# Kernel optimization log

Hardware: AMD Instinct MI355X
Metric: run time of the kernel (lower is better)

## Reference

```python
import jax, jax.numpy as jnp
import numpy as np

DIM = 1024
HEADS = 16
HEAD_DIM = DIM // HEADS
B, S = 4, 4096


def setup_inputs() -> dict:
    key = jax.random.key(0)
    ks = jax.random.split(key, 8)
    sc = 1.0 / np.sqrt(DIM)
    return {
        "x": jax.random.normal(ks[0], (B, S, DIM), dtype=jnp.float32),
        "Wq": jax.random.normal(ks[1], (DIM, DIM), dtype=jnp.float32) * sc,
        "Wk": jax.random.normal(ks[2], (DIM, DIM), dtype=jnp.float32) * sc,
        "Wv": jax.random.normal(ks[3], (DIM, DIM), dtype=jnp.float32) * sc,
        "Wp": jax.random.normal(ks[4], (DIM, DIM), dtype=jnp.float32) * sc,
        "bp": jnp.zeros((DIM,), dtype=jnp.float32),
        "conv_w": jax.random.normal(ks[5], (DIM, 3), dtype=jnp.float32) * (1.0 / np.sqrt(3.0)),
        "conv_b": jnp.zeros((DIM,), dtype=jnp.float32),
    }


def reference(x, Wq, Wk, Wv, Wp, bp, conv_w, conv_b):
    b, s, d = x.shape
    # projections -> [b, h, n, hd] (torch Linear: x @ W.T)
    def split_heads(t):
        return t.reshape(b, s, HEADS, HEAD_DIM).transpose(0, 2, 1, 3)
    q = split_heads(x @ Wq.T)
    k = split_heads(x @ Wk.T)
    v = split_heads(x @ Wv.T)
    # ELU(+1) feature map
    q = jax.nn.elu(q) + 1.0
    k = jax.nn.elu(k) + 1.0
    # global kv-state and k-state
    kv_state = jnp.einsum('bhnd,bhne->bhde', k, v)   # [b,h,hd,hd]
    k_state = k.sum(axis=2)                          # [b,h,hd]
    attn_out = jnp.einsum('bhnd,bhde->bhne', q, kv_state)
    denom = jnp.maximum(jnp.einsum('bhnd,bhd->bhn', q, k_state), 1e-6)[..., None]
    attn_out = (attn_out / denom).transpose(0, 2, 1, 3).reshape(b, s, d)
    # depthwise conv1d, kernel=3, padding=1 (per-channel)
    xp = jnp.pad(x, ((0, 0), (1, 1), (0, 0)))        # [b, s+2, d]
    local = (xp[:, :-2, :] * conv_w[:, 0]
             + xp[:, 1:-1, :] * conv_w[:, 1]
             + xp[:, 2:, :] * conv_w[:, 2]) + conv_b
    return (attn_out + local) @ Wp.T + bp
```

## Files before the change

kernel.cpp:

```cpp
#include <hip/hip_runtime.h>
#include <hip/hip_bf16.h>
#include <stdint.h>

#define DIMN 1024
#define HEADS 16
#define HD 64
#define BATCH 4
#define SEQ 4096
#define M_TOT (BATCH*SEQ)

typedef __attribute__((ext_vector_type(8))) __bf16 bf16x8;
typedef __attribute__((ext_vector_type(4))) __bf16 bf16x4;
typedef __attribute__((ext_vector_type(4))) float f32x4;

__device__ __forceinline__ void gload_lds16(const void* g, void* l) {
  __builtin_amdgcn_global_load_lds(
      (const __attribute__((address_space(1))) void*)(uintptr_t)g,
      (__attribute__((address_space(3))) void*)(uint32_t)(uintptr_t)l,
      16, 0, 0);
}

__device__ __forceinline__ uint32_t swz128(uint32_t off) {
  return off ^ (((off >> 7) & 7) << 4);
}

__device__ __forceinline__ void lfence() { asm volatile("" ::: "memory"); }
__device__ __forceinline__ void barx() { lfence(); __builtin_amdgcn_s_barrier(); lfence(); }

__global__ __launch_bounds__(256) void cast_x_kernel(const float* __restrict__ in,
                                                     __bf16* __restrict__ out, int n4) {
  int i = blockIdx.x * 256 + threadIdx.x;
  if (i < n4) {
    f32x4 v = ((const f32x4*)in)[i];
    bf16x4 o;
    o[0] = (__bf16)v[0]; o[1] = (__bf16)v[1]; o[2] = (__bf16)v[2]; o[3] = (__bf16)v[3];
    ((bf16x4*)out)[i] = o;
  }
}

__global__ __launch_bounds__(256) void cast_w4_kernel(const float* __restrict__ a,
                                                      const float* __restrict__ b,
                                                      const float* __restrict__ c,
                                                      const float* __restrict__ d,
                                                      __bf16* __restrict__ oa,
                                                      __bf16* __restrict__ ob,
                                                      __bf16* __restrict__ oc,
                                                      __bf16* __restrict__ od) {
  const float* srcs[4] = {a, b, c, d};
  __bf16* dsts[4] = {oa, ob, oc, od};
  const float* src = srcs[blockIdx.y];
  __bf16* dst = dsts[blockIdx.y];
  int i = blockIdx.x * 256 + threadIdx.x;
  f32x4 v = ((const f32x4*)src)[i];
  bf16x4 o;
  o[0] = (__bf16)v[0]; o[1] = (__bf16)v[1]; o[2] = (__bf16)v[2]; o[3] = (__bf16)v[3];
  ((bf16x4*)dst)[i] = o;
}

template <int MODE, int NT>
__global__ __launch_bounds__(512, 2) void gemm256(const __bf16* __restrict__ A,
                                                  const __bf16* __restrict__ Bw,
                                                  void* __restrict__ Cout,
                                                  const float* __restrict__ bias) {
  __shared__ char lds[131072];
  const int KB = DIMN * 2;
  const int NKT = DIMN / 64;
  const int bid = blockIdx.x;
  const int x = bid & 7, jj = bid >> 3;
  const int n_t = jj % NT, m_t = (jj / NT) * 8 + x;
  const int m0 = m_t * 256, n0 = n_t * 256;
  const int tid = threadIdx.x;
  const int lane = tid & 63;
  const int wave = tid >> 6;
  const int wm = wave >> 2;
  const int wn = wave & 3;
  const int r16 = lane & 15, r4 = lane >> 4;

  const uint32_t s_off0 = tid * 16;
  const uint32_t s_off1 = 8192 + tid * 16;
  const uint32_t s_row0 = s_off0 >> 7, s_row1 = s_off1 >> 7;
  const uint32_t s_col0 = (s_off0 ^ ((s_row0 & 7) << 4)) & 127;
  const uint32_t s_col1 = (s_off1 ^ ((s_row1 & 7) << 4)) & 127;

  const char* Ab = (const char*)A + (size_t)m0 * KB;
  const char* Bb = (const char*)Bw + (size_t)n0 * KB;

  auto STAGE = [&](int op, int h, int kt, int b) {
    const char* gb = (op ? Bb : Ab) + (size_t)(h * 128) * KB + kt * 128;
    char* lb = lds + op * 65536 + b * 32768 + h * 16384;
    gload_lds16(gb + s_row0 * KB + s_col0, lb + s_off0);
    gload_lds16(gb + s_row1 * KB + s_col1, lb + s_off1);
  };

  uint32_t axk[2];
#pragma unroll
  for (int k = 0; k < 2; ++k) axk[k] = (uint32_t)(k * 64 + r4 * 16) ^ ((r16 & 7) << 4);

  f32x4 acc[8][4] = {};
  bf16x8 bc[4][2];

  STAGE(1, 0, 0, 0); STAGE(1, 1, 0, 0); STAGE(0, 0, 0, 0); STAGE(0, 1, 0, 0);
  STAGE(1, 0, 1, 1); STAGE(1, 1, 1, 1); STAGE(0, 0, 1, 1);
  asm volatile("s_waitcnt vmcnt(6)" ::: "memory");
  barx();

  for (int kt = 0; kt < NKT; ++kt) {
    const int p = kt & 1;
    const char* abuf = lds + p * 32768;
    const char* bbuf = lds + 65536 + p * 32768;

    {
      bf16x8 af[2][2];
#pragma unroll
      for (int nf = 0; nf < 4; ++nf)
#pragma unroll
        for (int k = 0; k < 2; ++k)
          bc[nf][k] = *(const bf16x8*)(bbuf + (nf >> 1) * 16384 +
                        (((nf & 1) * 64 + wn * 16 + r16) << 7) + axk[k]);
#pragma unroll
      for (int i = 0; i < 2; ++i)
#pragma unroll
        for (int k = 0; k < 2; ++k)
          af[i][k] = *(const bf16x8*)(abuf + ((i * 32 + wm * 16 + r16) << 7) + axk[k]);
      if (kt + 1 < NKT) STAGE(0, 1, kt + 1, (kt + 1) & 1);
      barx();
      __builtin_amdgcn_s_setprio(1);
#pragma unroll
      for (int i = 0; i < 2; ++i)
#pragma unroll
        for (int nf = 0; nf < 4; ++nf)
#pragma unroll
          for (int k = 0; k < 2; ++k)
            acc[i][nf] = __builtin_amdgcn_mfma_f32_16x16x32_bf16(af[i][k], bc[nf][k], acc[i][nf], 0, 0, 0);
      __builtin_amdgcn_s_setprio(0);
      barx();
    }
    {
      bf16x8 af[2][2];
#pragma unroll
      for (int i = 0; i < 2; ++i)
#pragma unroll
        for (int k = 0; k < 2; ++k)
          af[i][k] = *(const bf16x8*)(abuf + (((2 + i) * 32 + wm * 16 + r16) << 7) + axk[k]);
      if (kt + 2 < NKT) STAGE(1, 0, kt + 2, p);
      barx();
      __builtin_amdgcn_s_setprio(1);
#pragma unroll
      for (int i = 0; i < 2; ++i)
#pragma unroll
        for (int nf = 0; nf < 4; ++nf)
#pragma unroll
          for (int k = 0; k < 2; ++k)
            acc[2 + i][nf] = __builtin_amdgcn_mfma_f32_16x16x32_bf16(af[i][k], bc[nf][k], acc[2 + i][nf], 0, 0, 0);
      __builtin_amdgcn_s_setprio(0);
      barx();
    }
    {
      bf16x8 af[2][2];
#pragma unroll
      for (int i = 0; i < 2; ++i)
#pragma unroll
        for (int k = 0; k < 2; ++k)
          af[i][k] = *(const bf16x8*)(abuf + 16384 + ((i * 32 + wm * 16 + r16) << 7) + axk[k]);
      if (kt + 2 < NKT) STAGE(1, 1, kt + 2, p);
      barx();
      __builtin_amdgcn_s_setprio(1);
#pragma unroll
      for (int i = 0; i < 2; ++i)
#pragma unroll
        for (int nf = 0; nf < 4; ++nf)
#pragma unroll
          for (int k = 0; k < 2; ++k)
            acc[4 + i][nf] = __builtin_amdgcn_mfma_f32_16x16x32_bf16(af[i][k], bc[nf][k], acc[4 + i][nf], 0, 0, 0);
      __builtin_amdgcn_s_setprio(0);
      barx();
    }
    {
      bf16x8 af[2][2];
#pragma unroll
      for (int i = 0; i < 2; ++i)
#pragma unroll
        for (int k = 0; k < 2; ++k)
          af[i][k] = *(const bf16x8*)(abuf + 16384 + (((2 + i) * 32 + wm * 16 + r16) << 7) + axk[k]);
      if (kt + 2 < NKT) STAGE(0, 0, kt + 2, p);
      if (kt == NKT - 2) { asm volatile("s_waitcnt vmcnt(0)" ::: "memory"); }
      else if (kt < NKT - 2) { asm volatile("s_waitcnt vmcnt(6)" ::: "memory"); }
      barx();
      __builtin_amdgcn_s_setprio(1);
#pragma unroll
      for (int i = 0; i < 2; ++i)
#pragma unroll
        for (int nf = 0; nf < 4; ++nf)
#pragma unroll
          for (int k = 0; k < 2; ++k)
            acc[6 + i][nf] = __builtin_amdgcn_mfma_f32_16x16x32_bf16(af[i][k], bc[nf][k], acc[6 + i][nf], 0, 0, 0);
      __builtin_amdgcn_s_setprio(0);
      barx();
    }
  }

#pragma unroll
  for (int mf = 0; mf < 8; ++mf) {
#pragma unroll
    for (int nf = 0; nf < 4; ++nf) {
#pragma unroll
      for (int r = 0; r < 4; ++r) {
        int row = m0 + mf * 32 + wm * 16 + r4 * 4 + r;
        int col = n0 + nf * 64 + wn * 16 + r16;
        float v = acc[mf][nf][r];
        if (MODE == 2) {
          ((float*)Cout)[(size_t)row * DIMN + col] = v + bias[col];
        } else {
          int wsel = col >> 10, c = col & 1023;
          if (wsel < 2) v = (v > 0.f) ? (v + 1.f) : __expf(v);
          int b = row >> 12, s = row & 4095;
          int h = c >> 6, e2 = c & 63;
          ((__bf16*)Cout)[(size_t)wsel * 16777216 +
                          ((size_t)((b * HEADS + h) * SEQ + s)) * HD + e2] = (__bf16)v;
        }
      }
    }
  }
}

__global__ __launch_bounds__(256) void kv_state_mfma(const __bf16* __restrict__ kp,
                                                     const __bf16* __restrict__ vb,
                                                     float* __restrict__ kv,
                                                     float* __restrict__ ks) {
  __shared__ __bf16 kt[64][136];
  __shared__ __bf16 vt[80][136];
  const int bid = blockIdx.x;
  const int bh = bid >> 2, nc = bid & 3;
  const int tid = threadIdx.x;
  const int lane = tid & 63;
  const int wave = tid >> 6;
  const int r16 = lane & 15, r4 = lane >> 4;

  for (int i = tid; i < 16 * 136; i += 256) {
    int rr = i / 136;
    vt[64 + rr][i - rr * 136] = (rr == 0) ? (__bf16)1.0f : (__bf16)0.0f;
  }

  const int trow = tid >> 1;
  const int tcol = (tid & 1) * 32;

  f32x4 acc[5] = {};
  bf16x8 kr[4], vr[4];

  size_t gb = ((size_t)bh * SEQ + nc * 1024 + trow) * HD + tcol;
#pragma unroll
  for (int q = 0; q < 4; ++q) {
    kr[q] = *(const bf16x8*)(kp + gb + q * 8);
    vr[q] = *(const bf16x8*)(vb + gb + q * 8);
  }

  for (int t = 0; t < 8; ++t) {
    __syncthreads();
#pragma unroll
    for (int q = 0; q < 4; ++q)
#pragma unroll
      for (int j = 0; j < 8; ++j) {
        kt[tcol + q * 8 + j][trow] = kr[q][j];
        vt[tcol + q * 8 + j][trow] = vr[q][j];
      }
    __syncthreads();
    if (t < 7) {
      size_t gb2 = ((size_t)bh * SEQ + nc * 1024 + (t + 1) * 128 + trow) * HD + tcol;
#pragma unroll
      for (int q = 0; q < 4; ++q) {
        kr[q] = *(const bf16x8*)(kp + gb2 + q * 8);
        vr[q] = *(const bf16x8*)(vb + gb2 + q * 8);
      }
    }
#pragma unroll
    for (int ksl = 0; ksl < 4; ++ksl) {
      bf16x8 af = *(const bf16x8*)&kt[wave * 16 + r16][ksl * 32 + r4 * 8];
#pragma unroll
      for (int eb = 0; eb < 5; ++eb) {
        bf16x8 bf_ = *(const bf16x8*)&vt[eb * 16 + r16][ksl * 32 + r4 * 8];
        acc[eb] = __builtin_amdgcn_mfma_f32_16x16x32_bf16(af, bf_, acc[eb], 0, 0, 0);
      }
    }
  }

#pragma unroll
  for (int eb = 0; eb < 4; ++eb)
#pragma unroll
    for (int r = 0; r < 4; ++r) {
      int d = wave * 16 + r4 * 4 + r;
      atomicAdd(&kv[(size_t)bh * 4096 + d * 64 + eb * 16 + r16], acc[eb][r]);
    }
  if (r16 == 0) {
#pragma unroll
    for (int r = 0; r < 4; ++r)
      atomicAdd(&ks[bh * 64 + wave * 16 + r4 * 4 + r], acc[4][r]);
  }
}

__global__ __launch_bounds__(256) void prep_kv_kernel(const float* __restrict__ kv,
                                                      const float* __restrict__ ks,
                                                      __bf16* __restrict__ kvb) {
  const int bh = blockIdx.x;
  const int tid = threadIdx.x;
  for (int idx = tid; idx < 80 * 64; idx += 256) {
    int e = idx >> 6, d = idx & 63;
    float v;
    if (e < 64)       v = kv[(size_t)bh * 4096 + d * 64 + e];
    else if (e == 64) v = ks[bh * 64 + d];
    else              v = 0.f;
    kvb[(size_t)bh * 5120 + idx] = (__bf16)v;
  }
}

__global__ __launch_bounds__(256) void attn_local_mfma(const __bf16* __restrict__ qp,
                                                       const __bf16* __restrict__ kvb,
                                                       const float* __restrict__ x,
                                                       const float* __restrict__ conv_w,
                                                       const float* __restrict__ conv_b,
                                                       __bf16* __restrict__ y) {
  __shared__ __bf16 qs[128 * 64];
  __shared__ __bf16 bs[80 * 64];
  const int bid = blockIdx.x;
  const int bh = bid >> 5;
  const int chunk = bid & 31;
  const int tid = threadIdx.x;
  const int lane = tid & 63;
  const int wave = tid >> 6;
  const int r16 = lane & 15, r4 = lane >> 4;

  const char* qbase  = (const char*)(qp + ((size_t)bh * SEQ + chunk * 128) * HD);
  const char* kvbase = (const char*)(kvb + (size_t)bh * 5120);
#pragma unroll
  for (int t = 0; t < 4; ++t) {
    int c = t * 4 + wave;
    uint32_t off = c * 1024 + lane * 16;
    gload_lds16(qbase + swz128(off), ((char*)qs) + off);
  }
#pragma unroll
  for (int t = 0; t < 3; ++t) {
    int c = t * 4 + wave;
    if (c < 10) {
      uint32_t off = c * 1024 + lane * 16;
      gload_lds16(kvbase + swz128(off), ((char*)bs) + off);
    }
  }
  __syncthreads();

  f32x4 acc[2][5] = {};
#pragma unroll
  for (int kstep = 0; kstep < 2; ++kstep) {
    bf16x8 af[2], bfr[5];
#pragma unroll
    for (int i = 0; i < 2; ++i) {
      uint32_t off = (wave * 32 + i * 16 + r16) * 128 + kstep * 64 + r4 * 16;
      af[i] = *(const bf16x8*)(((char*)qs) + swz128(off));
    }
#pragma unroll
    for (int j = 0; j < 5; ++j) {
      uint32_t off = (j * 16 + r16) * 128 + kstep * 64 + r4 * 16;
      bfr[j] = *(const bf16x8*)(((char*)bs) + swz128(off));
    }
#pragma unroll
    for (int i = 0; i < 2; ++i)
#pragma unroll
      for (int j = 0; j < 5; ++j)
        acc[i][j] = __builtin_amdgcn_mfma_f32_16x16x32_bf16(af[i], bfr[j], acc[i][j], 0, 0, 0);
  }

  const int b = bh >> 4, h = bh & 15;
  float w0[4], w1[4], w2[4], bb[4];
#pragma unroll
  for (int j = 0; j < 4; ++j) {
    int c = h * HD + j * 16 + r16;
    w0[j] = conv_w[c * 3 + 0]; w1[j] = conv_w[c * 3 + 1]; w2[j] = conv_w[c * 3 + 2];
    bb[j] = conv_b[c];
  }
#pragma unroll
  for (int i = 0; i < 2; ++i) {
#pragma unroll
    for (int r = 0; r < 4; ++r) {
      int s = chunk * 128 + wave * 32 + i * 16 + r4 * 4 + r;
      size_t m = (size_t)b * SEQ + s;
      float den = fmaxf(__shfl(acc[i][4][r], lane & 48), 1e-6f);
      float inv = 1.0f / den;
#pragma unroll
      for (int j = 0; j < 4; ++j) {
        int c = h * HD + j * 16 + r16;
        float xm = x[m * DIMN + c];
        float xl = (s > 0)       ? x[(m - 1) * DIMN + c] : 0.f;
        float xr = (s < SEQ - 1) ? x[(m + 1) * DIMN + c] : 0.f;
        float val = acc[i][j][r] * inv
                  + xl * w0[j] + xm * w1[j] + xr * w2[j] + bb[j];
        y[m * DIMN + c] = (__bf16)val;
      }
    }
  }
}

extern "C" void kernel_launch(void* const* d_in, const int* in_sizes, int n_in,
                              void* d_out, int out_size, void* d_ws, size_t ws_size,
                              hipStream_t stream) {
  const float* x  = (const float*)d_in[0];
  const float* Wq = (const float*)d_in[1];
  const float* Wk = (const float*)d_in[2];
  const float* Wv = (const float*)d_in[3];
  const float* Wp = (const float*)d_in[4];
  const float* bp = (const float*)d_in[5];
  const float* cw = (const float*)d_in[6];
  const float* cb = (const float*)d_in[7];
  float* out = (float*)d_out;

  char* ws = (char*)d_ws;
  const size_t MB = 1024 * 1024;
  __bf16* xb  = (__bf16*)(ws);
  __bf16* y   = xb;
  __bf16* qp  = (__bf16*)(ws + 32 * MB);
  __bf16* kp  = (__bf16*)(ws + 64 * MB);
  __bf16* vb  = (__bf16*)(ws + 96 * MB);
  __bf16* wqb = (__bf16*)(ws + 128 * MB);
  __bf16* wkb = (__bf16*)(ws + 130 * MB);
  __bf16* wvb = (__bf16*)(ws + 132 * MB);
  __bf16* wpb = (__bf16*)(ws + 134 * MB);
  float*  kv  = (float*)(ws + 136 * MB);
  float*  ks  = (float*)(ws + 137 * MB);
  __bf16* kvb = wqb;

  cast_x_kernel<<<M_TOT * DIMN / 4 / 256, 256, 0, stream>>>(x, xb, M_TOT * DIMN / 4);
  cast_w4_kernel<<<dim3(1024, 4), 256, 0, stream>>>(Wq, Wk, Wv, Wp, wqb, wkb, wvb, wpb);

  gemm256<3, 12><<<768, 512, 0, stream>>>(xb, wqb, qp, nullptr);

  hipMemsetAsync(kv, 0, 64 * 4096 * 4 + 64 * 64 * 4, stream);
  kv_state_mfma<<<256, 256, 0, stream>>>(kp, vb, kv, ks);
  prep_kv_kernel<<<64, 256, 0, stream>>>(kv, ks, kvb);

  attn_local_mfma<<<2048, 256, 0, stream>>>(qp, kvb, x, cw, cb, y);

  gemm256<2, 4><<<256, 512, 0, stream>>>(y, wpb, out, bp);
}
```

Baseline: 234.4 us.

## Swap MFMA operands for vectorized row-major epilogue stores and merge cast kernels

The GEMM MFMA operands are swapped so each lane's four accumulator values lie along consecutive output columns rather than rows. The epilogue can then write them as one 16-byte float4 store (with a vector bias load) or an 8-byte bf16x4 store, instead of four scalar stores. The ELU selection is hoisted to a per-tile check. Separately, the x and four weight cast kernels are merged into one launch to cut a kernel launch. Correctness depends on the transposed accumulator layout matching the new index math.

Result: slower. 241.5 us (+3.0%).

```diff
diff --git a/kernel.cpp b/kernel.cpp
--- a/kernel.cpp
+++ b/kernel.cpp
@@ -27,34 +27,31 @@
 __device__ __forceinline__ void lfence() { asm volatile("" ::: "memory"); }
 __device__ __forceinline__ void barx() { lfence(); __builtin_amdgcn_s_barrier(); lfence(); }
 
-__global__ __launch_bounds__(256) void cast_x_kernel(const float* __restrict__ in,
-                                                     __bf16* __restrict__ out, int n4) {
+__global__ __launch_bounds__(256) void cast_all_kernel(const float* __restrict__ x,
+                                                       const float* __restrict__ wq,
+                                                       const float* __restrict__ wk,
+                                                       const float* __restrict__ wv,
+                                                       const float* __restrict__ wp,
+                                                       __bf16* __restrict__ xb,
+                                                       __bf16* __restrict__ wqb,
+                                                       __bf16* __restrict__ wkb,
+                                                       __bf16* __restrict__ wvb,
+                                                       __bf16* __restrict__ wpb) {
   int i = blockIdx.x * 256 + threadIdx.x;
-  if (i < n4) {
-    f32x4 v = ((const f32x4*)in)[i];
-    bf16x4 o;
-    o[0] = (__bf16)v[0]; o[1] = (__bf16)v[1]; o[2] = (__bf16)v[2]; o[3] = (__bf16)v[3];
-    ((bf16x4*)out)[i] = o;
-  }
-}
-
-__global__ __launch_bounds__(256) void cast_w4_kernel(const float* __restrict__ a,
-                                                      const float* __restrict__ b,
-                                                      const float* __restrict__ c,
-                                                      const float* __restrict__ d,
-                                                      __bf16* __restrict__ oa,
-                                                      __bf16* __restrict__ ob,
-                                                      __bf16* __restrict__ oc,
-                                                      __bf16* __restrict__ od) {
-  const float* srcs[4] = {a, b, c, d};
-  __bf16* dsts[4] = {oa, ob, oc, od};
-  const float* src = srcs[blockIdx.y];
-  __bf16* dst = dsts[blockIdx.y];
-  int i = blockIdx.x * 256 + threadIdx.x;
-  f32x4 v = ((const f32x4*)src)[i];
+  const float* src; __bf16* dst; int j;
+  if (i < 4194304)      { src = x;  dst = xb;  j = i; }
+  else {
+    int t = i - 4194304;
+    int w = t >> 18; j = t & 262143;
+    if      (w == 0) { src = wq; dst = wqb; }
+    else if (w == 1) { src = wk; dst = wkb; }
+    else if (w == 2) { src = wv; dst = wvb; }
+    else             { src = wp; dst = wpb; }
+  }
+  f32x4 v = ((const f32x4*)src)[j];
   bf16x4 o;
   o[0] = (__bf16)v[0]; o[1] = (__bf16)v[1]; o[2] = (__bf16)v[2]; o[3] = (__bf16)v[3];
-  ((bf16x4*)dst)[i] = o;
+  ((bf16x4*)dst)[j] = o;
 }
 
 template <int MODE, int NT>
@@ -131,7 +128,7 @@
         for (int nf = 0; nf < 4; ++nf)
 #pragma unroll
           for (int k = 0; k < 2; ++k)
-            acc[i][nf] = __builtin_amdgcn_mfma_f32_16x16x32_bf16(af[i][k], bc[nf][k], acc[i][nf], 0, 0, 0);
+            acc[i][nf] = __builtin_amdgcn_mfma_f32_16x16x32_bf16(bc[nf][k], af[i][k], acc[i][nf], 0, 0, 0);
       __builtin_amdgcn_s_setprio(0);
       barx();
     }
@@ -151,7 +148,7 @@
         for (int nf = 0; nf < 4; ++nf)
 #pragma unroll
           for (int k = 0; k < 2; ++k)
-            acc[2 + i][nf] = __builtin_amdgcn_mfma_f32_16x16x32_bf16(af[i][k], bc[nf][k], acc[2 + i][nf], 0, 0, 0);
+            acc[2 + i][nf] = __builtin_amdgcn_mfma_f32_16x16x32_bf16(bc[nf][k], af[i][k], acc[2 + i][nf], 0, 0, 0);
       __builtin_amdgcn_s_setprio(0);
       barx();
     }
@@ -171,7 +168,7 @@
         for (int nf = 0; nf < 4; ++nf)
 #pragma unroll
           for (int k = 0; k < 2; ++k)
-            acc[4 + i][nf] = __builtin_amdgcn_mfma_f32_16x16x32_bf16(af[i][k], bc[nf][k], acc[4 + i][nf], 0, 0, 0);
+            acc[4 + i][nf] = __builtin_amdgcn_mfma_f32_16x16x32_bf16(bc[nf][k], af[i][k], acc[4 + i][nf], 0, 0, 0);
       __builtin_amdgcn_s_setprio(0);
       barx();
     }
@@ -193,31 +190,39 @@
         for (int nf = 0; nf < 4; ++nf)
 #pragma unroll
           for (int k = 0; k < 2; ++k)
-            acc[6 + i][nf] = __builtin_amdgcn_mfma_f32_16x16x32_bf16(af[i][k], bc[nf][k], acc[6 + i][nf], 0, 0, 0);
+            acc[6 + i][nf] = __builtin_amdgcn_mfma_f32_16x16x32_bf16(bc[nf][k], af[i][k], acc[6 + i][nf], 0, 0, 0);
       __builtin_amdgcn_s_setprio(0);
       barx();
     }
   }
 
+  const int wsel = n0 >> 10;
+  const bool do_elu = (MODE == 3) && (wsel < 2);
 #pragma unroll
   for (int mf = 0; mf < 8; ++mf) {
+    const int row = m0 + mf * 32 + wm * 16 + r16;
 #pragma unroll
     for (int nf = 0; nf < 4; ++nf) {
-#pragma unroll
-      for (int r = 0; r < 4; ++r) {
-        int row = m0 + mf * 32 + wm * 16 + r4 * 4 + r;
-        int col = n0 + nf * 64 + wn * 16 + r16;
-        float v = acc[mf][nf][r];
-        if (MODE == 2) {
-          ((float*)Cout)[(size_t)row * DIMN + col] = v + bias[col];
-        } else {
-          int wsel = col >> 10, c = col & 1023;
-          if (wsel < 2) v = (v > 0.f) ? (v + 1.f) : __expf(v);
-          int b = row >> 12, s = row & 4095;
-          int h = c >> 6, e2 = c & 63;
-          ((__bf16*)Cout)[(size_t)wsel * 16777216 +
-                          ((size_t)((b * HEADS + h) * SEQ + s)) * HD + e2] = (__bf16)v;
+      const int n = n0 + nf * 64 + wn * 16 + r4 * 4;
+      if (MODE == 2) {
+        f32x4 bq = *(const f32x4*)(bias + n);
+        f32x4 o;
+#pragma unroll
+        for (int r = 0; r < 4; ++r) o[r] = acc[mf][nf][r] + bq[r];
+        *(f32x4*)&((float*)Cout)[(size_t)row * DIMN + n] = o;
+      } else {
+        bf16x4 o;
+#pragma unroll
+        for (int r = 0; r < 4; ++r) {
+          float v = acc[mf][nf][r];
+          if (do_elu) v = (v > 0.f) ? (v + 1.f) : __expf(v);
+          o[r] = (__bf16)v;
         }
+        int c = n & 1023;
+        int h = c >> 6, e2 = c & 63;
+        int b = row >> 12, s = row & 4095;
+        *(bf16x4*)&((__bf16*)Cout)[(size_t)wsel * 16777216 +
+                    ((size_t)((b * HEADS + h) * SEQ + s)) * HD + e2] = o;
       }
     }
   }
@@ -425,8 +430,7 @@
   float*  ks  = (float*)(ws + 137 * MB);
   __bf16* kvb = wqb;
 
-  cast_x_kernel<<<M_TOT * DIMN / 4 / 256, 256, 0, stream>>>(x, xb, M_TOT * DIMN / 4);
-  cast_w4_kernel<<<dim3(1024, 4), 256, 0, stream>>>(Wq, Wk, Wv, Wp, wqb, wkb, wvb, wpb);
+  cast_all_kernel<<<20480, 256, 0, stream>>>(x, Wq, Wk, Wv, Wp, xb, wqb, wkb, wvb, wpb);
 
   gemm256<3, 12><<<768, 512, 0, stream>>>(xb, wqb, qp, nullptr);
 
```
